# Kernel tuning notes

Hardware: AMD Instinct MI355X
Metric: run time of the kernel (lower is better)

The kernel has to match this reference:

```python
import jax, jax.numpy as jnp
import numpy as np

ALPHA = 1.0
LAMBDA_ADV = 0.5
MARGIN = 0.5
EPS = 1e-8  # torch F.cosine_similarity eps


def setup_inputs() -> dict:
    key = jax.random.key(0)
    k1, k2, k3 = jax.random.split(key, 3)
    B, D, C = 8192, 1024, 1000
    features = jax.random.normal(k1, (B, D), dtype=jnp.float32)
    labels = jax.random.randint(k2, (B,), 0, C, dtype=jnp.int64)
    centers = jax.random.normal(k3, (C, D), dtype=jnp.float32)
    return {"features": features, "labels": labels, "centers": centers}


def reference(features, labels, centers):
    # --- intra-class term: gather centers, cosine-decayed MSE ---
    cb = centers[labels]                                   # [B, D]
    f_norm = jnp.maximum(jnp.linalg.norm(features, axis=1), EPS)   # [B]
    c_norm = jnp.maximum(jnp.linalg.norm(cb, axis=1), EPS)         # [B]
    sim = jnp.sum(features * cb, axis=1) / (f_norm * c_norm)       # [B]
    sq_err = jnp.sum((features - cb) ** 2, axis=1)                 # [B]
    intra_loss = jnp.mean(sq_err / jnp.exp(ALPHA * sim))

    # --- adversarial term: pairwise cosine sim as normalize + GEMM ---
    fhat = features / f_norm[:, None]                       # [B, D]
    sim_matrix = fhat @ fhat.T                              # [B, B]
    mask = labels[:, None] != labels[None, :]               # [B, B] bool
    hinge = jnp.where(mask, jax.nn.relu(MARGIN - sim_matrix), 0.0)
    n_pairs = jnp.maximum(jnp.sum(mask), 1).astype(hinge.dtype)
    adv_loss = jnp.sum(hinge) / n_pairs

    return intra_loss + LAMBDA_ADV * adv_loss
```

## Files before the change

kernel.cpp:

```cpp
#include <hip/hip_runtime.h>


typedef __attribute__((ext_vector_type(8))) short bf16x8;
typedef __attribute__((ext_vector_type(4))) float f32x4;

#define NROWS 8192
#define NDIM  1024
#define NCLS  1000
#define NTILE 32
#define NTRI  528

#define FHAT_OFF  0
#define INTRA_OFF 16777216
#define ADV_OFF   (INTRA_OFF + NROWS * 4)
#define HIST_OFF  (ADV_OFF + NTRI * 4)
#define WS_NEEDED (HIST_OFF + NCLS * 4)

static __device__ __forceinline__ unsigned short f2bf(float x) {
  unsigned u = __float_as_uint(x);
  u += 0x7fffu + ((u >> 16) & 1u);
  return (unsigned short)(u >> 16);
}

__global__ __launch_bounds__(256) void prep_kernel(
    const float* __restrict__ feat, const int* __restrict__ labels,
    const float* __restrict__ centers, unsigned short* __restrict__ fhat,
    float* __restrict__ intra_val, int* __restrict__ hist) {
  const int tid = threadIdx.x, wave = tid >> 6, lane = tid & 63;
  const int row = blockIdx.x * 4 + wave;

  const float4* fr = (const float4*)(feat + (size_t)row * NDIM);
  const int lab = labels[row];
  const float4* cr = (const float4*)(centers + (size_t)lab * NDIM);

  float4 f[4], c[4];
  #pragma unroll
  for (int j = 0; j < 4; ++j) { f[j] = fr[lane + j * 64]; c[j] = cr[lane + j * 64]; }

  float ff = 0.f, fc = 0.f, cc = 0.f, se = 0.f;
  #pragma unroll
  for (int j = 0; j < 4; ++j) {
    ff += f[j].x*f[j].x + f[j].y*f[j].y + f[j].z*f[j].z + f[j].w*f[j].w;
    fc += f[j].x*c[j].x + f[j].y*c[j].y + f[j].z*c[j].z + f[j].w*c[j].w;
    cc += c[j].x*c[j].x + c[j].y*c[j].y + c[j].z*c[j].z + c[j].w*c[j].w;
    float dx = f[j].x-c[j].x, dy = f[j].y-c[j].y, dz = f[j].z-c[j].z, dw = f[j].w-c[j].w;
    se += dx*dx + dy*dy + dz*dz + dw*dw;
  }
  #pragma unroll
  for (int off = 1; off < 64; off <<= 1) {
    ff += __shfl_xor(ff, off, 64);
    fc += __shfl_xor(fc, off, 64);
    cc += __shfl_xor(cc, off, 64);
    se += __shfl_xor(se, off, 64);
  }
  const float fn = fmaxf(sqrtf(ff), 1e-8f);
  const float cn = fmaxf(sqrtf(cc), 1e-8f);
  const float inv = 1.0f / fn;
  if (lane == 0) {
    intra_val[row] = se * expf(-(fc / (fn * cn)));
    atomicAdd(&hist[lab], 1);
  }
  ushort4* orow = (ushort4*)(fhat + (size_t)row * NDIM);
  #pragma unroll
  for (int j = 0; j < 4; ++j) {
    ushort4 o;
    o.x = f2bf(f[j].x * inv); o.y = f2bf(f[j].y * inv);
    o.z = f2bf(f[j].z * inv); o.w = f2bf(f[j].w * inv);
    orow[lane + j * 64] = o;
  }
}

#define CUMUL(r) ((r) * NTILE - (r) * ((r) - 1) / 2)

__global__ __launch_bounds__(512) void gemm_hinge_kernel(
    const unsigned short* __restrict__ fhat, const int* __restrict__ labels,
    float* __restrict__ adv_val) {
  const int bid0 = blockIdx.x;
  const int bid  = (bid0 & 7) * 66 + (bid0 >> 3);
  const float nf = (float)NTILE + 0.5f;
  int ti = (int)floorf(nf - sqrtf(nf * nf - 2.0f * (float)bid));
  while (ti > 0 && bid < CUMUL(ti)) --ti;
  while (bid >= CUMUL(ti + 1)) ++ti;
  const int tj = ti + (bid - CUMUL(ti));

  __shared__ __align__(16) unsigned short Al[2][256 * 64];
  __shared__ __align__(16) unsigned short Bl[2][256 * 64];
  __shared__ int labi[256], labj[256];
  __shared__ float rsum[8];

  const int tid  = threadIdx.x;
  const int wave = tid >> 6, lane = tid & 63;
  const int wr = wave >> 2, wc = wave & 3;

  if (tid < 256) labi[tid] = labels[ti * 256 + tid];
  else           labj[tid - 256] = labels[tj * 256 + (tid - 256)];

  f32x4 acc[8][4] = {};

  const int l8 = lane >> 3;
  const int sl = ((lane & 7) ^ l8) * 8;
  const unsigned short* aS = fhat + (size_t)(ti * 256 + wave * 32 + l8) * NDIM + sl;
  const unsigned short* bS = fhat + (size_t)(tj * 256 + wave * 32 + l8) * NDIM + sl;

#define STAGE(BUF, K0)                                                        \
  do {                                                                        \
    _Pragma("unroll")                                                         \
    for (int j = 0; j < 4; ++j) {                                             \
      __builtin_amdgcn_global_load_lds(                                       \
          (const __attribute__((address_space(1))) void*)(aS + (K0) + j * 8 * NDIM), \
          (__attribute__((address_space(3))) void*)&Al[BUF][(wave * 4 + j) * 512],   \
          16, 0, 0);                                                          \
      __builtin_amdgcn_global_load_lds(                                       \
          (const __attribute__((address_space(1))) void*)(bS + (K0) + j * 8 * NDIM), \
          (__attribute__((address_space(3))) void*)&Bl[BUF][(wave * 4 + j) * 512],   \
          16, 0, 0);                                                          \
    }                                                                         \
  } while (0)

  const int lr = lane & 15;
  const int hk = (lane >> 4) * 8;
  const int xr = (lr & 7) << 3;

#define COMPUTE(BUF)                                                          \
  do {                                                                        \
    _Pragma("unroll")                                                         \
    for (int kk = 0; kk < 2; ++kk) {                                          \
      const int lk = kk * 32 + hk;                                            \
      const int lx = lk ^ xr;                                                 \
      bf16x8 a[8], b[4];                                                      \
      _Pragma("unroll")                                                       \
      for (int m = 0; m < 8; ++m)                                             \
        a[m] = *(const bf16x8*)&Al[BUF][(wr * 128 + m * 16 + lr) * 64 + lx];  \
      _Pragma("unroll")                                                       \
      for (int n = 0; n < 4; ++n)                                             \
        b[n] = *(const bf16x8*)&Bl[BUF][(wc * 64 + n * 16 + lr) * 64 + lx];   \
      _Pragma("unroll")                                                       \
      for (int m = 0; m < 8; ++m)                                             \
        _Pragma("unroll")                                                     \
        for (int n = 0; n < 4; ++n)                                           \
          acc[m][n] = __builtin_amdgcn_mfma_f32_16x16x32_bf16(                \
              a[m], b[n], acc[m][n], 0, 0, 0);                                \
    }                                                                         \
  } while (0)

#define KITER(T, CBUF)                                                        \
  do {                                                                        \
    STAGE(CBUF ^ 1, ((T) + 1) * 64);                                          \
    __builtin_amdgcn_sched_barrier(0);                                        \
    asm volatile("s_waitcnt vmcnt(8)" ::: "memory");                          \
    __builtin_amdgcn_sched_barrier(0);                                        \
    __builtin_amdgcn_s_barrier();                                             \
    __builtin_amdgcn_sched_barrier(0);                                        \
    COMPUTE(CBUF);                                                            \
    asm volatile("s_waitcnt lgkmcnt(0)" ::: "memory");                        \
    __builtin_amdgcn_sched_barrier(0);                                        \
    __builtin_amdgcn_s_barrier();                                             \
    __builtin_amdgcn_sched_barrier(0);                                        \
  } while (0)

  STAGE(0, 0);
  #pragma unroll 1
  for (int t2 = 0; t2 < 7; ++t2) {
    KITER(2 * t2, 0);
    KITER(2 * t2 + 1, 1);
  }
  KITER(14, 0);
  asm volatile("s_waitcnt vmcnt(0)" ::: "memory");
  __builtin_amdgcn_sched_barrier(0);
  __builtin_amdgcn_s_barrier();
  __builtin_amdgcn_sched_barrier(0);
  COMPUTE(1);

#undef KITER
#undef STAGE
#undef COMPUTE

  float hs = 0.f;
  const int crow = (lane >> 4) * 4;
  const int ccol = lane & 15;
  #pragma unroll
  for (int m = 0; m < 8; ++m) {
    #pragma unroll
    for (int n = 0; n < 4; ++n) {
      #pragma unroll
      for (int r = 0; r < 4; ++r) {
        const int i = wr * 128 + m * 16 + crow + r;
        const int j = wc * 64 + n * 16 + ccol;
        if (labi[i] != labj[j]) {
          hs += fmaxf(0.5f - acc[m][n][r], 0.f);
        }
      }
    }
  }
  #pragma unroll
  for (int off = 32; off; off >>= 1) hs += __shfl_down(hs, off, 64);
  if (lane == 0) rsum[wave] = hs;
  __syncthreads();
  if (tid == 0) {
    float s = 0.f;
    #pragma unroll
    for (int w = 0; w < 8; ++w) s += rsum[w];
    if (ti != tj) s *= 2.f;
    adv_val[bid0] = s;
  }
}

__global__ __launch_bounds__(1024) void finalize_kernel(
    const float* __restrict__ intra_val, const float* __restrict__ adv_val,
    const int* __restrict__ hist, float* __restrict__ out) {
  __shared__ float rsi[16], rsa[16];
  __shared__ long long rsq[16];
  const int tid = threadIdx.x;
  const int wave = tid >> 6, lane = tid & 63;

  float si = 0.f;
  for (int i = tid; i < NROWS; i += 1024) si += intra_val[i];
  float sa = 0.f;
  if (tid < NTRI) sa = adv_val[tid];
  long long sq = 0;
  if (tid < NCLS) { long long h = hist[tid]; sq = h * h; }

  #pragma unroll
  for (int off = 32; off; off >>= 1) {
    si += __shfl_down(si, off, 64);
    sa += __shfl_down(sa, off, 64);
    sq += __shfl_down(sq, off, 64);
  }
  if (lane == 0) { rsi[wave] = si; rsa[wave] = sa; rsq[wave] = sq; }
  __syncthreads();
  if (tid == 0) {
    float SI = 0.f, SA = 0.f; long long SQ = 0;
    for (int w = 0; w < 16; ++w) { SI += rsi[w]; SA += rsa[w]; SQ += rsq[w]; }
    long long npairs = (long long)NROWS * NROWS - SQ;
    if (npairs < 1) npairs = 1;
    out[0] = SI / (float)NROWS + 0.5f * (SA / (float)npairs);
  }
}

__global__ void sentinel_kernel(float* out) {
  if (threadIdx.x == 0 && blockIdx.x == 0) out[0] = -1.0f;
}

extern "C" void kernel_launch(void* const* d_in, const int* in_sizes, int n_in,
                              void* d_out, int out_size, void* d_ws, size_t ws_size,
                              hipStream_t stream) {
  const float* feat    = (const float*)d_in[0];
  const int*   labels  = (const int*)d_in[1];
  const float* centers = (const float*)d_in[2];
  float* out = (float*)d_out;

  if (ws_size < (size_t)WS_NEEDED) {
    sentinel_kernel<<<1, 64, 0, stream>>>(out);
    return;
  }

  char* ws = (char*)d_ws;
  unsigned short* fhat = (unsigned short*)(ws + FHAT_OFF);
  float* intra_val = (float*)(ws + INTRA_OFF);
  float* adv_val   = (float*)(ws + ADV_OFF);
  int*   hist      = (int*)(ws + HIST_OFF);

  hipMemsetAsync(ws + HIST_OFF, 0, NCLS * 4, stream);

  prep_kernel<<<NROWS / 4, 256, 0, stream>>>(feat, labels, centers, fhat,
                                             intra_val, hist);
  gemm_hinge_kernel<<<NTRI, 512, 0, stream>>>(fhat, labels, adv_val);
  finalize_kernel<<<1, 1024, 0, stream>>>(intra_val, adv_val, hist, out);
}
```

Before: 182.0 us.

## Split GEMM tail: 512 full tiles plus 16 tiles as quarter blocks

The 528 upper-triangular 256x256 tiles are now split across two launches. 512 full tiles run in one kernel. The remaining 16 tiles are cut into 128x128 quarters and handled by 64 blocks in a second kernel. This targets the wave-quantization tail on 256 CUs, where 528 blocks leave a partial second wave. It also raises wave priority during the MFMA compute sections. The cost is an extra kernel launch serialized on the stream, and the quarter kernel has lower per-block efficiency.

After: 170.9 us. -6.1%, faster.

```diff
diff --git a/kernel.cpp b/kernel.cpp
--- a/kernel.cpp
+++ b/kernel.cpp
@@ -8,12 +8,12 @@
 #define NDIM  1024
 #define NCLS  1000
 #define NTILE 32
-#define NTRI  528
+#define NADV  576
 
 #define FHAT_OFF  0
 #define INTRA_OFF 16777216
 #define ADV_OFF   (INTRA_OFF + NROWS * 4)
-#define HIST_OFF  (ADV_OFF + NTRI * 4)
+#define HIST_OFF  (ADV_OFF + NADV * 4)
 #define WS_NEEDED (HIST_OFF + NCLS * 4)
 
 static __device__ __forceinline__ unsigned short f2bf(float x) {
@@ -72,16 +72,19 @@
 
 #define CUMUL(r) ((r) * NTILE - (r) * ((r) - 1) / 2)
 
-__global__ __launch_bounds__(512) void gemm_hinge_kernel(
+#define TRI_DECODE(BID, TI, TJ)                                               \
+  const float nf = (float)NTILE + 0.5f;                                       \
+  int TI = (int)floorf(nf - sqrtf(nf * nf - 2.0f * (float)(BID)));            \
+  while (TI > 0 && (BID) < CUMUL(TI)) --TI;                                   \
+  while ((BID) >= CUMUL(TI + 1)) ++TI;                                        \
+  const int TJ = TI + ((BID) - CUMUL(TI));
+
+__global__ __launch_bounds__(512) void gemm_full_kernel(
     const unsigned short* __restrict__ fhat, const int* __restrict__ labels,
     float* __restrict__ adv_val) {
-  const int bid0 = blockIdx.x;
-  const int bid  = (bid0 & 7) * 66 + (bid0 >> 3);
-  const float nf = (float)NTILE + 0.5f;
-  int ti = (int)floorf(nf - sqrtf(nf * nf - 2.0f * (float)bid));
-  while (ti > 0 && bid < CUMUL(ti)) --ti;
-  while (bid >= CUMUL(ti + 1)) ++ti;
-  const int tj = ti + (bid - CUMUL(ti));
+  const int f = blockIdx.x;
+  const int bid = (f & 7) * 66 + (f >> 3);
+  TRI_DECODE(bid, ti, tj);
 
   __shared__ __align__(16) unsigned short Al[2][256 * 64];
   __shared__ __align__(16) unsigned short Bl[2][256 * 64];
@@ -123,10 +126,10 @@
 
 #define COMPUTE(BUF)                                                          \
   do {                                                                        \
+    __builtin_amdgcn_s_setprio(1);                                            \
     _Pragma("unroll")                                                         \
     for (int kk = 0; kk < 2; ++kk) {                                          \
-      const int lk = kk * 32 + hk;                                            \
-      const int lx = lk ^ xr;                                                 \
+      const int lx = (kk * 32 + hk) ^ xr;                                     \
       bf16x8 a[8], b[4];                                                      \
       _Pragma("unroll")                                                       \
       for (int m = 0; m < 8; ++m)                                             \
@@ -141,6 +144,7 @@
           acc[m][n] = __builtin_amdgcn_mfma_f32_16x16x32_bf16(                \
               a[m], b[n], acc[m][n], 0, 0, 0);                                \
     }                                                                         \
+    __builtin_amdgcn_s_setprio(0);                                            \
   } while (0)
 
 #define KITER(T, CBUF)                                                        \
@@ -179,19 +183,15 @@
   const int crow = (lane >> 4) * 4;
   const int ccol = lane & 15;
   #pragma unroll
-  for (int m = 0; m < 8; ++m) {
+  for (int m = 0; m < 8; ++m)
     #pragma unroll
-    for (int n = 0; n < 4; ++n) {
+    for (int n = 0; n < 4; ++n)
       #pragma unroll
       for (int r = 0; r < 4; ++r) {
         const int i = wr * 128 + m * 16 + crow + r;
         const int j = wc * 64 + n * 16 + ccol;
-        if (labi[i] != labj[j]) {
-          hs += fmaxf(0.5f - acc[m][n][r], 0.f);
-        }
+        if (labi[i] != labj[j]) hs += fmaxf(0.5f - acc[m][n][r], 0.f);
       }
-    }
-  }
   #pragma unroll
   for (int off = 32; off; off >>= 1) hs += __shfl_down(hs, off, 64);
   if (lane == 0) rsum[wave] = hs;
@@ -201,7 +201,137 @@
     #pragma unroll
     for (int w = 0; w < 8; ++w) s += rsum[w];
     if (ti != tj) s *= 2.f;
-    adv_val[bid0] = s;
+    adv_val[f] = s;
+  }
+}
+
+__global__ __launch_bounds__(512) void gemm_quarter_kernel(
+    const unsigned short* __restrict__ fhat, const int* __restrict__ labels,
+    float* __restrict__ adv_val) {
+  const int bq = blockIdx.x;
+  const int p = bq >> 2;
+  const int bid = (p >> 1) * 66 + 64 + (p & 1);
+  const int qm = (bq >> 1) & 1, qn = bq & 1;
+  TRI_DECODE(bid, ti, tj);
+  const int row0 = ti * 256 + qm * 128;
+  const int col0 = tj * 256 + qn * 128;
+
+  __shared__ __align__(16) unsigned short Al[2][128 * 64];
+  __shared__ __align__(16) unsigned short Bl[2][128 * 64];
+  __shared__ int labi[128], labj[128];
+  __shared__ float rsum[8];
+
+  const int tid  = threadIdx.x;
+  const int wave = tid >> 6, lane = tid & 63;
+  const int wr = wave >> 2, wc = wave & 3;
+
+  if (tid < 128) labi[tid] = labels[row0 + tid];
+  else if (tid < 256) labj[tid - 128] = labels[col0 + (tid - 128)];
+
+  f32x4 acc[4][2] = {};
+
+  const int l8 = lane >> 3;
+  const int sl = ((lane & 7) ^ l8) * 8;
+  const unsigned short* aS = fhat + (size_t)(row0 + wave * 16 + l8) * NDIM + sl;
+  const unsigned short* bS = fhat + (size_t)(col0 + wave * 16 + l8) * NDIM + sl;
+
+#define STAGE(BUF, K0)                                                        \
+  do {                                                                        \
+    _Pragma("unroll")                                                         \
+    for (int j = 0; j < 2; ++j) {                                             \
+      __builtin_amdgcn_global_load_lds(                                       \
+          (const __attribute__((address_space(1))) void*)(aS + (K0) + j * 8 * NDIM), \
+          (__attribute__((address_space(3))) void*)&Al[BUF][(wave * 2 + j) * 512],   \
+          16, 0, 0);                                                          \
+      __builtin_amdgcn_global_load_lds(                                       \
+          (const __attribute__((address_space(1))) void*)(bS + (K0) + j * 8 * NDIM), \
+          (__attribute__((address_space(3))) void*)&Bl[BUF][(wave * 2 + j) * 512],   \
+          16, 0, 0);                                                          \
+    }                                                                         \
+  } while (0)
+
+  const int lr = lane & 15;
+  const int hk = (lane >> 4) * 8;
+  const int xr = (lr & 7) << 3;
+
+#define COMPUTE(BUF)                                                          \
+  do {                                                                        \
+    __builtin_amdgcn_s_setprio(1);                                            \
+    _Pragma("unroll")                                                         \
+    for (int kk = 0; kk < 2; ++kk) {                                          \
+      const int lx = (kk * 32 + hk) ^ xr;                                     \
+      bf16x8 a[4], b[2];                                                      \
+      _Pragma("unroll")                                                       \
+      for (int m = 0; m < 4; ++m)                                             \
+        a[m] = *(const bf16x8*)&Al[BUF][(wr * 64 + m * 16 + lr) * 64 + lx];   \
+      _Pragma("unroll")                                                       \
+      for (int n = 0; n < 2; ++n)                                             \
+        b[n] = *(const bf16x8*)&Bl[BUF][(wc * 32 + n * 16 + lr) * 64 + lx];   \
+      _Pragma("unroll")                                                       \
+      for (int m = 0; m < 4; ++m)                                             \
+        _Pragma("unroll")                                                     \
+        for (int n = 0; n < 2; ++n)                                           \
+          acc[m][n] = __builtin_amdgcn_mfma_f32_16x16x32_bf16(                \
+              a[m], b[n], acc[m][n], 0, 0, 0);                                \
+    }                                                                         \
+    __builtin_amdgcn_s_setprio(0);                                            \
+  } while (0)
+
+#define KITER(T, CBUF)                                                        \
+  do {                                                                        \
+    STAGE(CBUF ^ 1, ((T) + 1) * 64);                                          \
+    __builtin_amdgcn_sched_barrier(0);                                        \
+    asm volatile("s_waitcnt vmcnt(4)" ::: "memory");                          \
+    __builtin_amdgcn_sched_barrier(0);                                        \
+    __builtin_amdgcn_s_barrier();                                             \
+    __builtin_amdgcn_sched_barrier(0);                                        \
+    COMPUTE(CBUF);                                                            \
+    asm volatile("s_waitcnt lgkmcnt(0)" ::: "memory");                        \
+    __builtin_amdgcn_sched_barrier(0);                                        \
+    __builtin_amdgcn_s_barrier();                                             \
+    __builtin_amdgcn_sched_barrier(0);                                        \
+  } while (0)
+
+  STAGE(0, 0);
+  #pragma unroll 1
+  for (int t2 = 0; t2 < 7; ++t2) {
+    KITER(2 * t2, 0);
+    KITER(2 * t2 + 1, 1);
+  }
+  KITER(14, 0);
+  asm volatile("s_waitcnt vmcnt(0)" ::: "memory");
+  __builtin_amdgcn_sched_barrier(0);
+  __builtin_amdgcn_s_barrier();
+  __builtin_amdgcn_sched_barrier(0);
+  COMPUTE(1);
+
+#undef KITER
+#undef STAGE
+#undef COMPUTE
+
+  float hs = 0.f;
+  const int crow = (lane >> 4) * 4;
+  const int ccol = lane & 15;
+  #pragma unroll
+  for (int m = 0; m < 4; ++m)
+    #pragma unroll
+    for (int n = 0; n < 2; ++n)
+      #pragma unroll
+      for (int r = 0; r < 4; ++r) {
+        const int i = wr * 64 + m * 16 + crow + r;
+        const int j = wc * 32 + n * 16 + ccol;
+        if (labi[i] != labj[j]) hs += fmaxf(0.5f - acc[m][n][r], 0.f);
+      }
+  #pragma unroll
+  for (int off = 32; off; off >>= 1) hs += __shfl_down(hs, off, 64);
+  if (lane == 0) rsum[wave] = hs;
+  __syncthreads();
+  if (tid == 0) {
+    float s = 0.f;
+    #pragma unroll
+    for (int w = 0; w < 8; ++w) s += rsum[w];
+    if (ti != tj) s *= 2.f;
+    adv_val[512 + bq] = s;
   }
 }
 
@@ -216,7 +346,7 @@
   float si = 0.f;
   for (int i = tid; i < NROWS; i += 1024) si += intra_val[i];
   float sa = 0.f;
-  if (tid < NTRI) sa = adv_val[tid];
+  if (tid < NADV) sa = adv_val[tid];
   long long sq = 0;
   if (tid < NCLS) { long long h = hist[tid]; sq = h * h; }
 
@@ -264,6 +394,7 @@
 
   prep_kernel<<<NROWS / 4, 256, 0, stream>>>(feat, labels, centers, fhat,
                                              intra_val, hist);
-  gemm_hinge_kernel<<<NTRI, 512, 0, stream>>>(fhat, labels, adv_val);
+  gemm_full_kernel<<<512, 512, 0, stream>>>(fhat, labels, adv_val);
+  gemm_quarter_kernel<<<64, 512, 0, stream>>>(fhat, labels, adv_val);
   finalize_kernel<<<1, 1024, 0, stream>>>(intra_val, adv_val, hist, out);
 }
```
